# Kernel tuning notes

Measured on AMD Instinct MI355X. Metric: run time of the kernel, lower is better.

Reference implementation:

```python
import jax, jax.numpy as jnp
import numpy as np

B, N, E = 256, 256, 512
ITER = 10

def setup_inputs() -> dict:
    key = jax.random.key(0)
    k1, k2, k3 = jax.random.split(key, 3)
    feats = jax.random.normal(k1, (B, N, E), dtype=jnp.float32)
    logits = jax.random.normal(k2, (B, N, 1), dtype=jnp.float32)
    # nn.Parameter initialized to zeros in the original; use small random values
    # so the CRF update is non-trivial for correctness checking.
    W = jax.random.normal(k3, (1, N, N), dtype=jnp.float32) * 0.01
    return {"feats": feats, "logits": logits, "W": W}

def reference(feats, logits, W):
    # cosine similarity between all node pairs: [B, N, N]
    feats_norm = jnp.linalg.norm(feats, axis=2, keepdims=True)          # [B,N,1]
    pairwise_norm = feats_norm @ jnp.swapaxes(feats_norm, 1, 2)         # [B,N,N]
    pairwise_dot = jnp.einsum('bne,bme->bnm', feats, feats)             # [B,N,N]
    pairwise_sim = pairwise_dot / pairwise_norm
    W_sym = (W + jnp.swapaxes(W, 1, 2)) * 0.5                           # [1,N,N]
    pairwise_potential = pairwise_sim * W_sym                           # [B,N,N]
    unary_potential = logits                                            # [B,N,1]

    def step(lg, _):
        probs = jnp.swapaxes(jax.nn.sigmoid(lg), 1, 2)                  # [B,1,N]
        # probs*P - (1-probs)*P == (2*probs - 1)*P
        e = jnp.sum((2.0 * probs - 1.0) * pairwise_potential,
                    axis=2, keepdims=True)                              # [B,N,1]
        return unary_potential + e, None

    out, _ = jax.lax.scan(step, logits, None, length=ITER)
    return out
```

## Files before the change

kernel.cpp:

```cpp
#include <hip/hip_runtime.h>
#include <hip/hip_bf16.h>
#include <math.h>

#define Bb   256
#define Nn   256
#define Ee   512
#define TKF  64
#define NCH  (Ee / TKF)
#define NITER 10

typedef __attribute__((ext_vector_type(8))) short bf16x8;
typedef __attribute__((ext_vector_type(4))) float f32x4;

typedef __attribute__((address_space(1))) const void glb_cv;
typedef __attribute__((address_space(3))) void lds_v;

static __device__ __forceinline__ unsigned short f2bf(float f) {
    __hip_bfloat16 h = __float2bfloat16(f);
    return __builtin_bit_cast(unsigned short, h);
}

static __device__ __forceinline__ bf16x8 ldfrag(const unsigned char* bt, int row, int ks, int hi) {
    const int byte = row * 128 + (((ks * 64 + hi * 16)) ^ ((row & 7) << 4));
    return *reinterpret_cast<const bf16x8*>(bt + byte);
}

__global__ __launch_bounds__(256) void wsym_k(const float* __restrict__ W,
                                              float* __restrict__ wsym) {
    const int idx = blockIdx.x * 256 + threadIdx.x;
    const int r  = idx >> 6;
    const int c0 = (idx & 63) * 4;
    const float4 a = *reinterpret_cast<const float4*>(&W[r * Nn + c0]);
    float4 o;
    o.x = 0.5f * (a.x + W[(c0 + 0) * Nn + r]);
    o.y = 0.5f * (a.y + W[(c0 + 1) * Nn + r]);
    o.z = 0.5f * (a.z + W[(c0 + 2) * Nn + r]);
    o.w = 0.5f * (a.w + W[(c0 + 3) * Nn + r]);
    *reinterpret_cast<float4*>(&wsym[r * Nn + c0]) = o;
}

template <bool USE_WS>
__global__ __launch_bounds__(512, 2) void crf_mfma(
    const float* __restrict__ feats,
    const float* __restrict__ logits,
    const float* __restrict__ W,
    const float* __restrict__ wsym,
    float* __restrict__ out)
{
    const int b    = blockIdx.x;
    const int t    = threadIdx.x;
    const int wave = t >> 6;
    const int lane = t & 63;
    const int wr   = wave >> 1;
    const int wc   = wave & 1;
    const int lo   = lane & 15;
    const int hi   = lane >> 4;

    __shared__ float fstage[Nn * TKF];
    __shared__ unsigned char btile[Nn * 128];
    __shared__ float invn[Nn];
    __shared__ float svec[Nn];
    __shared__ float uvec[Nn];
    __shared__ float lgv[Nn];
    __shared__ float part[4][Nn];

    f32x4 acc[4][8];
#pragma unroll
    for (int i = 0; i < 4; ++i)
#pragma unroll
        for (int j = 0; j < 8; ++j) acc[i][j] = (f32x4){0.f, 0.f, 0.f, 0.f};

    const float* Fb = feats + (size_t)b * Nn * Ee;

    auto stage = [&](int ch) {
#pragma unroll
        for (int i = 0; i < 8; ++i) {
            const int r0s = wave * 32 + i * 4;
            const int row = r0s + (lane >> 4);
            const float* src = Fb + (size_t)row * Ee + ch * TKF + (lane & 15) * 4;
            __builtin_amdgcn_global_load_lds((glb_cv*)src,
                                             (lds_v*)(fstage + r0s * TKF), 16, 0, 0);
        }
    };

    auto convert = [&]() {
#pragma unroll
        for (int g = 0; g < 8; ++g) {
            const int m   = t + 512 * g;
            const int row = m >> 4;
            const int gc  = m & 15;
            const float4 v = *reinterpret_cast<const float4*>(fstage + m * 4);
            ushort4 pk;
            pk.x = f2bf(v.x); pk.y = f2bf(v.y); pk.z = f2bf(v.z); pk.w = f2bf(v.w);
            *reinterpret_cast<ushort4*>(
                btile + row * 128 + ((gc * 8) ^ ((row & 7) << 4))) = pk;
        }
    };

    stage(0);
    if (t < Nn) {
        const float u = logits[(size_t)b * Nn + t];
        uvec[t] = u;
        lgv[t]  = u;
    }
    __syncthreads();

    for (int ch = 0; ch < NCH; ++ch) {
        convert();
        __syncthreads();
        if (ch + 1 < NCH) stage(ch + 1);
#pragma unroll
        for (int ks = 0; ks < 2; ++ks) {
            bf16x8 af[4];
#pragma unroll
            for (int rb = 0; rb < 4; ++rb)
                af[rb] = ldfrag(btile, wr * 64 + rb * 16 + lo, ks, hi);
#pragma unroll
            for (int cg = 0; cg < 2; ++cg) {
                bf16x8 bfv[4];
#pragma unroll
                for (int cq = 0; cq < 4; ++cq)
                    bfv[cq] = ldfrag(btile, wc * 128 + (cg * 4 + cq) * 16 + lo, ks, hi);
#pragma unroll
                for (int rb = 0; rb < 4; ++rb)
#pragma unroll
                    for (int cq = 0; cq < 4; ++cq)
                        acc[rb][cg * 4 + cq] = __builtin_amdgcn_mfma_f32_16x16x32_bf16(
                            af[rb], bfv[cq], acc[rb][cg * 4 + cq], 0, 0, 0);
            }
        }
        __syncthreads();
    }

#pragma unroll
    for (int rb = 0; rb < 4; ++rb) {
        const int rowbase = wr * 64 + rb * 16;
#pragma unroll
        for (int cb = 0; cb < 8; ++cb) {
            const int colbase = wc * 128 + cb * 16;
            if (rowbase == colbase) {
#pragma unroll
                for (int r = 0; r < 4; ++r) {
                    if (hi * 4 + r == lo)
                        invn[rowbase + hi * 4 + r] = 1.0f / sqrtf(acc[rb][cb][r]);
                }
            }
        }
    }
    __syncthreads();

#pragma unroll
    for (int rb = 0; rb < 4; ++rb) {
        const int rbase = wr * 64 + rb * 16 + hi * 4;
        const float4 ir4 = *reinterpret_cast<const float4*>(&invn[rbase]);
        const float ir[4] = {ir4.x, ir4.y, ir4.z, ir4.w};
#pragma unroll
        for (int cb = 0; cb < 8; ++cb) {
            const int col = wc * 128 + cb * 16 + lo;
            const float ic = invn[col];
            if (USE_WS) {
#pragma unroll
                for (int r = 0; r < 4; ++r) {
                    const float ws = wsym[(rbase + r) * Nn + col];
                    acc[rb][cb][r] = acc[rb][cb][r] * ir[r] * ic * ws;
                }
            } else {
                const float4 wt = *reinterpret_cast<const float4*>(&W[col * Nn + rbase]);
                const float wtr[4] = {wt.x, wt.y, wt.z, wt.w};
#pragma unroll
                for (int r = 0; r < 4; ++r) {
                    const float ws = 0.5f * (W[(rbase + r) * Nn + col] + wtr[r]);
                    acc[rb][cb][r] = acc[rb][cb][r] * ir[r] * ic * ws;
                }
            }
        }
    }

    for (int itr = 0; itr < NITER; ++itr) {
        if (t < Nn) {
            const float x = lgv[t];
            svec[t] = 2.f / (1.f + __expf(-x)) - 1.f;
        }
        __syncthreads();

        float ep[8] = {0.f, 0.f, 0.f, 0.f, 0.f, 0.f, 0.f, 0.f};
#pragma unroll
        for (int rb = 0; rb < 4; ++rb) {
            const float4 s4 = *reinterpret_cast<const float4*>(
                &svec[wr * 64 + rb * 16 + hi * 4]);
#pragma unroll
            for (int cb = 0; cb < 8; ++cb)
                ep[cb] += acc[rb][cb][0] * s4.x + acc[rb][cb][1] * s4.y
                        + acc[rb][cb][2] * s4.z + acc[rb][cb][3] * s4.w;
        }
#pragma unroll
        for (int cb = 0; cb < 8; ++cb) {
            ep[cb] += __shfl_xor(ep[cb], 16);
            ep[cb] += __shfl_xor(ep[cb], 32);
        }
        if (lane < 16) {
#pragma unroll
            for (int cb = 0; cb < 8; ++cb)
                part[wr][wc * 128 + cb * 16 + lane] = ep[cb];
        }
        __syncthreads();
        if (t < Nn)
            lgv[t] = uvec[t] + part[0][t] + part[1][t] + part[2][t] + part[3][t];
    }

    if (t < Nn) out[(size_t)b * Nn + t] = lgv[t];
}

extern "C" void kernel_launch(void* const* d_in, const int* in_sizes, int n_in,
                              void* d_out, int out_size, void* d_ws, size_t ws_size,
                              hipStream_t stream) {
    const float* feats  = (const float*)d_in[0];
    const float* logits = (const float*)d_in[1];
    const float* W      = (const float*)d_in[2];
    float* out = (float*)d_out;

    if (ws_size >= (size_t)Nn * Nn * sizeof(float)) {
        float* wsym = (float*)d_ws;
        wsym_k<<<dim3(64), dim3(256), 0, stream>>>(W, wsym);
        crf_mfma<true><<<dim3(Bb), dim3(512), 0, stream>>>(feats, logits, W, wsym, out);
    } else {
        crf_mfma<false><<<dim3(Bb), dim3(512), 0, stream>>>(feats, logits, W, nullptr, out);
    }
}
```

Baseline: 48.67 us.

## Double-buffer feature staging with smaller K chunks and manual waitcnt barriers

```diff
diff --git a/kernel.cpp b/kernel.cpp
--- a/kernel.cpp
+++ b/kernel.cpp
@@ -5,7 +5,7 @@
 #define Bb   256
 #define Nn   256
 #define Ee   512
-#define TKF  64
+#define TKF  32
 #define NCH  (Ee / TKF)
 #define NITER 10
 
@@ -14,14 +14,17 @@
 
 typedef __attribute__((address_space(1))) const void glb_cv;
 typedef __attribute__((address_space(3))) void lds_v;
+
+#define VMCNT(n) asm volatile("s_waitcnt vmcnt(" #n ")" ::: "memory")
+#define LGKM0()  asm volatile("s_waitcnt lgkmcnt(0)" ::: "memory")
 
 static __device__ __forceinline__ unsigned short f2bf(float f) {
     __hip_bfloat16 h = __float2bfloat16(f);
     return __builtin_bit_cast(unsigned short, h);
 }
 
-static __device__ __forceinline__ bf16x8 ldfrag(const unsigned char* bt, int row, int ks, int hi) {
-    const int byte = row * 128 + (((ks * 64 + hi * 16)) ^ ((row & 7) << 4));
+static __device__ __forceinline__ bf16x8 ldfrag(const unsigned char* bt, int row, int hi) {
+    const int byte = row * 64 + ((hi * 16) ^ ((row & 3) << 4));
     return *reinterpret_cast<const bf16x8*>(bt + byte);
 }
 
@@ -56,8 +59,8 @@
     const int lo   = lane & 15;
     const int hi   = lane >> 4;
 
-    __shared__ float fstage[Nn * TKF];
-    __shared__ unsigned char btile[Nn * 128];
+    __shared__ float fstage[2][Nn * TKF];
+    __shared__ unsigned char btile[2][Nn * 64];
     __shared__ float invn[Nn];
     __shared__ float svec[Nn];
     __shared__ float uvec[Nn];
@@ -72,64 +75,70 @@
 
     const float* Fb = feats + (size_t)b * Nn * Ee;
 
-    auto stage = [&](int ch) {
-#pragma unroll
-        for (int i = 0; i < 8; ++i) {
-            const int r0s = wave * 32 + i * 4;
-            const int row = r0s + (lane >> 4);
-            const float* src = Fb + (size_t)row * Ee + ch * TKF + (lane & 15) * 4;
+    auto stage = [&](int ch, int buf) {
+#pragma unroll
+        for (int i = 0; i < 4; ++i) {
+            const int gbase = wave * 4 + i;
+            const int row   = gbase * 8 + (lane >> 3);
+            const float* src = Fb + (size_t)row * Ee + ch * TKF + (lane & 7) * 4;
             __builtin_amdgcn_global_load_lds((glb_cv*)src,
-                                             (lds_v*)(fstage + r0s * TKF), 16, 0, 0);
+                                             (lds_v*)(&fstage[buf][gbase * 256]), 16, 0, 0);
         }
     };
 
-    auto convert = [&]() {
-#pragma unroll
-        for (int g = 0; g < 8; ++g) {
+    auto convert = [&](int buf) {
+#pragma unroll
+        for (int g = 0; g < 4; ++g) {
             const int m   = t + 512 * g;
-            const int row = m >> 4;
-            const int gc  = m & 15;
-            const float4 v = *reinterpret_cast<const float4*>(fstage + m * 4);
+            const int row = m >> 3;
+            const int gc  = m & 7;
+            const float4 v = *reinterpret_cast<const float4*>(&fstage[buf][m * 4]);
             ushort4 pk;
             pk.x = f2bf(v.x); pk.y = f2bf(v.y); pk.z = f2bf(v.z); pk.w = f2bf(v.w);
             *reinterpret_cast<ushort4*>(
-                btile + row * 128 + ((gc * 8) ^ ((row & 7) << 4))) = pk;
+                &btile[buf][row * 64 + ((gc * 8) ^ ((row & 3) << 4))]) = pk;
         }
     };
 
-    stage(0);
+    auto mfma_step = [&](int buf) {
+        const unsigned char* tb = &btile[buf][0];
+        bf16x8 af[4];
+#pragma unroll
+        for (int rb = 0; rb < 4; ++rb)
+            af[rb] = ldfrag(tb, wr * 64 + rb * 16 + lo, hi);
+#pragma unroll
+        for (int cg = 0; cg < 2; ++cg) {
+            bf16x8 bfv[4];
+#pragma unroll
+            for (int cq = 0; cq < 4; ++cq)
+                bfv[cq] = ldfrag(tb, wc * 128 + (cg * 4 + cq) * 16 + lo, hi);
+#pragma unroll
+            for (int rb = 0; rb < 4; ++rb)
+#pragma unroll
+                for (int cq = 0; cq < 4; ++cq)
+                    acc[rb][cg * 4 + cq] = __builtin_amdgcn_mfma_f32_16x16x32_bf16(
+                        af[rb], bfv[cq], acc[rb][cg * 4 + cq], 0, 0, 0);
+        }
+    };
+
+    float uval = 0.f;
+    if (t < Nn) uval = logits[(size_t)b * Nn + t];
+    stage(0, 0);
+    stage(1, 1);
     if (t < Nn) {
-        const float u = logits[(size_t)b * Nn + t];
-        uvec[t] = u;
-        lgv[t]  = u;
-    }
-    __syncthreads();
-
+        uvec[t] = uval;
+        lgv[t]  = uval;
+    }
+
+#pragma unroll 2
     for (int ch = 0; ch < NCH; ++ch) {
-        convert();
-        __syncthreads();
-        if (ch + 1 < NCH) stage(ch + 1);
-#pragma unroll
-        for (int ks = 0; ks < 2; ++ks) {
-            bf16x8 af[4];
-#pragma unroll
-            for (int rb = 0; rb < 4; ++rb)
-                af[rb] = ldfrag(btile, wr * 64 + rb * 16 + lo, ks, hi);
-#pragma unroll
-            for (int cg = 0; cg < 2; ++cg) {
-                bf16x8 bfv[4];
-#pragma unroll
-                for (int cq = 0; cq < 4; ++cq)
-                    bfv[cq] = ldfrag(btile, wc * 128 + (cg * 4 + cq) * 16 + lo, ks, hi);
-#pragma unroll
-                for (int rb = 0; rb < 4; ++rb)
-#pragma unroll
-                    for (int cq = 0; cq < 4; ++cq)
-                        acc[rb][cg * 4 + cq] = __builtin_amdgcn_mfma_f32_16x16x32_bf16(
-                            af[rb], bfv[cq], acc[rb][cg * 4 + cq], 0, 0, 0);
-            }
-        }
-        __syncthreads();
+        if (ch + 1 < NCH) { VMCNT(4); } else { VMCNT(0); }
+        __builtin_amdgcn_s_barrier();
+        convert(ch & 1);
+        LGKM0();
+        __builtin_amdgcn_s_barrier();
+        if (ch + 2 < NCH) stage(ch + 2, ch & 1);
+        mfma_step(ch & 1);
     }
 
 #pragma unroll
```

New measurement: 45.69 us (median of 2 runs). 1.07x faster.
